# Kernel optimization log

Hardware: AMD Instinct MI355X
Metric: run time of the kernel (lower is better)

The kernel has to match this reference:

```python
import jax, jax.numpy as jnp
import numpy as np
import math

HIDDEN = 256

def setup_inputs() -> dict:
    key = jax.random.key(0)
    ks = jax.random.split(key, 4)
    x = jax.random.normal(ks[0], (64, 1024, 32), dtype=jnp.float32)
    Wq = jax.random.normal(ks[1], (32, HIDDEN), dtype=jnp.float32) * (1.0 / math.sqrt(32))
    Wk = jax.random.normal(ks[2], (32, HIDDEN), dtype=jnp.float32) * (1.0 / math.sqrt(32))
    Wv = jax.random.normal(ks[3], (32, HIDDEN), dtype=jnp.float32) * (1.0 / math.sqrt(32))
    bq = jnp.zeros((HIDDEN,), jnp.float32)
    bk = jnp.zeros((HIDDEN,), jnp.float32)
    bv = jnp.zeros((HIDDEN,), jnp.float32)
    return {"x": x, "Wq": Wq, "bq": bq, "Wk": Wk, "bk": bk, "Wv": Wv, "bv": bv}

def reference(x, Wq, bq, Wk, bk, Wv, bv):
    # per-sample single-head attention; softmax FIRST, then divide by sqrt(hidden)
    Q = jnp.einsum('bsi,ih->bsh', x, Wq) + bq  # [B,S,H]
    K = jnp.einsum('bsi,ih->bsh', x, Wk) + bk
    V = jnp.einsum('bsi,ih->bsh', x, Wv) + bv
    scores = jnp.einsum('bqh,bkh->bqk', Q, K)  # [B,S,S]
    attn = jax.nn.softmax(scores, axis=-1) / jnp.sqrt(jnp.float32(Q.shape[-1]))
    Z = jnp.einsum('bqk,bkh->bqh', attn, V)
    return Z
```

## Files before the change

### kernel.cpp

```cpp
#include <hip/hip_runtime.h>
#include <math.h>

#define NB   64
#define SEQ  1024
#define DIN  32
#define HID  256
#define QT   128
#define KT   64
#define NKT  (SEQ/KT)

typedef float        f32x16 __attribute__((ext_vector_type(16)));
typedef short        s16x8  __attribute__((ext_vector_type(8)));
typedef _Float16     f16x8  __attribute__((ext_vector_type(8)));
typedef unsigned int u32x4v __attribute__((ext_vector_type(4)));
typedef unsigned int u32x2v __attribute__((ext_vector_type(2)));

#define MFMA32(A,B,C)  __builtin_amdgcn_mfma_f32_32x32x16_bf16(A,B,C,0,0,0)
#define MFMA32H(A,B,C) __builtin_amdgcn_mfma_f32_32x32x16_f16(A,B,C,0,0,0)

#define OFF_WVT  4224
#define OFF_A    24576
#define OFF_T    (OFF_A + 64*16*8192)
#define WS_NEED  ((size_t)OFF_T + 64*16*4096)

#define SETB(g,p) (((g)*2+(p))*12288)
#define ATS_OFF   49152
#define SMEM_SZ   (ATS_OFF + 4224)

__device__ __forceinline__ unsigned pk_bf16(float lo, float hi) {
  unsigned r;
  asm("v_cvt_pk_bf16_f32 %0, %1, %2" : "=v"(r) : "v"(lo), "v"(hi));
  return r;
}
__device__ __forceinline__ unsigned pkh(float a, float b) {
  return __builtin_bit_cast(unsigned, __builtin_amdgcn_cvt_pkrtz(a, b));
}
__device__ __forceinline__ void plswap(unsigned &vdst, unsigned &vsrc) {
  u32x2v r = __builtin_amdgcn_permlane32_swap(vdst, vsrc, false, false);
  vdst = r[0]; vsrc = r[1];
}
__device__ __forceinline__ float cross_max(float v) {
  u32x2v r = __builtin_amdgcn_permlane32_swap(__float_as_uint(v), __float_as_uint(v), false, false);
  return fmaxf(__uint_as_float(r[0]), __uint_as_float(r[1]));
}
__device__ __forceinline__ float cross_add(float v) {
  u32x2v r = __builtin_amdgcn_permlane32_swap(__float_as_uint(v), __float_as_uint(v), false, false);
  return __uint_as_float(r[0]) + __uint_as_float(r[1]);
}
__device__ __forceinline__ s16x8 frag4(unsigned a, unsigned b, unsigned c, unsigned d) {
  u32x4v t; t[0]=a; t[1]=b; t[2]=c; t[3]=d;
  return __builtin_bit_cast(s16x8, t);
}
__device__ __forceinline__ f16x8 frag4h(unsigned a, unsigned b, unsigned c, unsigned d) {
  u32x4v t; t[0]=a; t[1]=b; t[2]=c; t[3]=d;
  return __builtin_bit_cast(f16x8, t);
}
__device__ __forceinline__ f16x8 ldh(const void* p) {
  return __builtin_bit_cast(f16x8, *(const u32x4v*)p);
}
__device__ __forceinline__ unsigned bf16_hi_bits(float f) {
  unsigned ux = __float_as_uint(f);
  return (ux + 0x7fffu + ((ux >> 16) & 1u)) >> 16;
}
__device__ __forceinline__ unsigned pack_h2(float a, float b) {
  _Float16 ha = (_Float16)a, hb = (_Float16)b;
  return (unsigned)__builtin_bit_cast(unsigned short, ha) |
         ((unsigned)__builtin_bit_cast(unsigned short, hb) << 16);
}


__global__ __launch_bounds__(256) void pack2_kernel(
    const float* __restrict__ x,
    const float* __restrict__ Wq, const float* __restrict__ Wk,
    const float* __restrict__ bq, const float* __restrict__ Wv,
    char* __restrict__ ws) {
  __shared__ float xs[64 * 33];
  const int bid = blockIdx.x;
  const int t   = threadIdx.x;
  if (bid < 1024) {
    const int b = bid >> 4, kt = bid & 15;
    {
      const int r = t >> 2, c = (t & 3) * 8;
      const float* src = x + ((size_t)(b*SEQ + kt*KT + r))*DIN + c;
      float4 v0 = *(const float4*)src, v1 = *(const float4*)(src + 4);
      float* d = xs + r*33 + c;
      d[0]=v0.x; d[1]=v0.y; d[2]=v0.z; d[3]=v0.w;
      d[4]=v1.x; d[5]=v1.y; d[6]=v1.z; d[7]=v1.w;
    }
    __syncthreads();
    const int l = t & 63, f = t >> 6;
    const int w = l >> 5, lq = l & 31;
    {
      const int row = ((f&2)?32:0) + lq;
      const int d0  = ((f&1)?16:0) + 8*w;
      const float* vsrc = xs + row*33 + d0;
      unsigned hi[4], lo[4];
      #pragma unroll
      for (int j = 0; j < 4; ++j) {
        float a = vsrc[2*j], c2 = vsrc[2*j+1];
        _Float16 ha = (_Float16)a, hb = (_Float16)c2;
        hi[j] = (unsigned)__builtin_bit_cast(unsigned short, ha) |
                ((unsigned)__builtin_bit_cast(unsigned short, hb) << 16);
        lo[j] = pack_h2(a - (float)ha, c2 - (float)hb);
      }
      char* dst = ws + OFF_A + (size_t)bid*8192 + f*1024 + l*16;
      *(u32x4v*)dst          = (u32x4v){hi[0],hi[1],hi[2],hi[3]};
      *(u32x4v*)(dst + 4096) = (u32x4v){lo[0],lo[1],lo[2],lo[3]};
    }
    {
      const int k0 = 16*f + 8*w;
      unsigned hi[4];
      #pragma unroll
      for (int j = 0; j < 4; ++j)
        hi[j] = pack_h2(xs[(k0 + 2*j)*33 + lq], xs[(k0 + 2*j + 1)*33 + lq]);
      char* dst = ws + OFF_T + (size_t)bid*4096 + f*1024 + l*16;
      *(u32x4v*)dst = (u32x4v){hi[0],hi[1],hi[2],hi[3]};
    }
  } else {
    const int gid = (bid - 1024) * 256 + t;
    float* wsf = (float*)ws;
    if (gid < 1024) {
      int i = gid >> 5, j = gid & 31;
      const float* a  = Wq + j * HID;
      const float* b2 = Wk + i * HID;
      float a0=0.f,a1=0.f,a2=0.f,a3=0.f;
      for (int h = 0; h < HID; h += 8) {
        float4 x1 = *(const float4*)(a + h),  y1 = *(const float4*)(b2 + h);
        float4 x2 = *(const float4*)(a + h+4), y2 = *(const float4*)(b2 + h+4);
        a0 = fmaf(x1.x,y1.x,a0); a1 = fmaf(x1.y,y1.y,a1);
        a2 = fmaf(x1.z,y1.z,a2); a3 = fmaf(x1.w,y1.w,a3);
        a0 = fmaf(x2.x,y2.x,a0); a1 = fmaf(x2.y,y2.y,a1);
        a2 = fmaf(x2.z,y2.z,a2); a3 = fmaf(x2.w,y2.w,a3);
      }
      wsf[gid] = (a0+a1)+(a2+a3);
    } else if (gid < 1056) {
      int i2 = gid - 1024;
      const float* b2 = Wk + i2 * HID;
      float acc = 0.f;
      for (int h = 0; h < HID; ++h) acc = fmaf(b2[h], bq[h], acc);
      wsf[1024 + i2] = acc;
    } else if (gid < 1056 + HID*16) {
      int e = gid - 1056;
      int h = e >> 4, d = e & 15;
      ((unsigned*)(ws + OFF_WVT))[e] = pkh(Wv[(2*d)*HID + h], Wv[(2*d+1)*HID + h]);
    }
  }
}

__global__ __launch_bounds__(512, 4) void attn_fast(
    const float* __restrict__ x, const char* __restrict__ ws,
    const float* __restrict__ bv, float* __restrict__ out) {
  __shared__ __align__(16) char smem[40960];
  const int bid = blockIdx.x;
  const int vid = (bid & 7) * 128 + (bid >> 3);
  const int b   = vid >> 4;
  const int q0  = (vid & 15) * 64;
  const int t = threadIdx.x;
  const int wid = t>>6, lane = t&63, w = lane>>5, lq = lane&31;
  const int grp = wid >> 1, wq = wid & 1;

  float* ATs = (float*)smem;
  {
    const float* wsf = (const float*)ws;
    for (int e = t; e < 1056; e += 512) ATs[e] = wsf[e];
  }
  __syncthreads();
  f16x8 G0h, G0l, G1h, G1l;
  {
    float xq[32];
    const float* xrow = x + (size_t)(b*SEQ + q0 + wq*32 + lq) * DIN;
    #pragma unroll
    for (int c = 0; c < 8; ++c) {
      float4 v = *(const float4*)(xrow + c*4);
      xq[c*4+0]=v.x; xq[c*4+1]=v.y; xq[c*4+2]=v.z; xq[c*4+3]=v.w;
    }
    float g[16];
    #pragma unroll
    for (int ii = 0; ii < 16; ++ii) {
      const int i = 8*w + 16*(ii>>3) + (ii&7);
      const float* ar = ATs + i*32;
      float acc = ATs[1024 + i];
      #pragma unroll
      for (int j = 0; j < 8; ++j) {
        float4 av = *(const float4*)(ar + j*4);
        acc = fmaf(xq[j*4+0], av.x, acc);
        acc = fmaf(xq[j*4+1], av.y, acc);
        acc = fmaf(xq[j*4+2], av.z, acc);
        acc = fmaf(xq[j*4+3], av.w, acc);
      }
      g[ii] = acc;
    }
    __syncthreads();
    unsigned gh[8], gl[8];
    #pragma unroll
    for (int p = 0; p < 8; ++p) {
      float a = g[2*p], bb = g[2*p+1];
      _Float16 ha = (_Float16)a, hb = (_Float16)bb;
      gh[p] = (unsigned)__builtin_bit_cast(unsigned short, ha) |
              ((unsigned)__builtin_bit_cast(unsigned short, hb) << 16);
      gl[p] = pack_h2(a - (float)ha, bb - (float)hb);
    }
    G0h = frag4h(gh[0],gh[1],gh[2],gh[3]);
    G1h = frag4h(gh[4],gh[5],gh[6],gh[7]);
    G0l = frag4h(gl[0],gl[1],gl[2],gl[3]);
    G1l = frag4h(gl[4],gl[5],gl[6],gl[7]);
  }

  f32x16 oacc;
  #pragma unroll
  for (int r = 0; r < 16; ++r) oacc[r] = 0.f;
  float m = -INFINITY, l = 0.f;

  const char* Ab = ws + OFF_A + (size_t)(b*16 + grp*4)*8192;
  const char* Tb = ws + OFF_T + (size_t)(b*16 + grp*4)*4096;
  const int lo16 = lane*16;

  #pragma unroll 2
  for (int j = 0; j < 4; ++j) {
    const char* A = Ab + j*8192;
    const char* T = Tb + j*4096;
    f16x8 ah0 = ldh(A + 0*1024 + lo16);
    f16x8 ah1 = ldh(A + 1*1024 + lo16);
    f16x8 ah2 = ldh(A + 2*1024 + lo16);
    f16x8 ah3 = ldh(A + 3*1024 + lo16);
    f16x8 al0 = ldh(A + 4096 + 0*1024 + lo16);
    f16x8 al1 = ldh(A + 4096 + 1*1024 + lo16);
    f16x8 al2 = ldh(A + 4096 + 2*1024 + lo16);
    f16x8 al3 = ldh(A + 4096 + 3*1024 + lo16);
    f16x8 at0 = ldh(T + 0*1024 + lo16);
    f16x8 at1 = ldh(T + 1*1024 + lo16);
    f16x8 at2 = ldh(T + 2*1024 + lo16);
    f16x8 at3 = ldh(T + 3*1024 + lo16);

    f32x16 sa0, sa1;
    #pragma unroll
    for (int r = 0; r < 16; ++r) { sa0[r] = 0.f; sa1[r] = 0.f; }
    sa0 = MFMA32H(ah0, G0h, sa0); sa0 = MFMA32H(ah0, G0l, sa0); sa0 = MFMA32H(al0, G0h, sa0);
    sa0 = MFMA32H(ah1, G1h, sa0); sa0 = MFMA32H(ah1, G1l, sa0); sa0 = MFMA32H(al1, G1h, sa0);
    sa1 = MFMA32H(ah2, G0h, sa1); sa1 = MFMA32H(ah2, G0l, sa1); sa1 = MFMA32H(al2, G0h, sa1);
    sa1 = MFMA32H(ah3, G1h, sa1); sa1 = MFMA32H(ah3, G1l, sa1); sa1 = MFMA32H(al3, G1h, sa1);

    float t0 = fmaxf(fmaxf(sa0[0], sa0[1]),  fmaxf(sa0[2],  sa0[3]));
    float t1 = fmaxf(fmaxf(sa0[4], sa0[5]),  fmaxf(sa0[6],  sa0[7]));
    float t2 = fmaxf(fmaxf(sa0[8], sa0[9]),  fmaxf(sa0[10], sa0[11]));
    float t3 = fmaxf(fmaxf(sa0[12],sa0[13]), fmaxf(sa0[14], sa0[15]));
    float t4 = fmaxf(fmaxf(sa1[0], sa1[1]),  fmaxf(sa1[2],  sa1[3]));
    float t5 = fmaxf(fmaxf(sa1[4], sa1[5]),  fmaxf(sa1[6],  sa1[7]));
    float t6 = fmaxf(fmaxf(sa1[8], sa1[9]),  fmaxf(sa1[10], sa1[11]));
    float t7 = fmaxf(fmaxf(sa1[12],sa1[13]), fmaxf(sa1[14], sa1[15]));
    float tm = fmaxf(fmaxf(fmaxf(t0,t1), fmaxf(t2,t3)),
                     fmaxf(fmaxf(t4,t5), fmaxf(t6,t7)));
    tm = cross_max(tm);
    if (!__all(tm - m <= 8.0f)) {
      float mn = fmaxf(m, tm);
      float alpha = __expf(m - mn);
      m = mn;
      l *= alpha;
      #pragma unroll
      for (int r = 0; r < 16; ++r) oacc[r] *= alpha;
    }
    #pragma unroll
    for (int r = 0; r < 16; ++r) { sa0[r] = __expf(sa0[r] - m); sa1[r] = __expf(sa1[r] - m); }
    float s0 = (sa0[0] + sa0[1])  + (sa0[2]  + sa0[3]);
    float s1 = (sa0[4] + sa0[5])  + (sa0[6]  + sa0[7]);
    float s2 = (sa0[8] + sa0[9])  + (sa0[10] + sa0[11]);
    float s3 = (sa0[12]+ sa0[13]) + (sa0[14] + sa0[15]);
    float s4 = (sa1[0] + sa1[1])  + (sa1[2]  + sa1[3]);
    float s5 = (sa1[4] + sa1[5])  + (sa1[6]  + sa1[7]);
    float s6 = (sa1[8] + sa1[9])  + (sa1[10] + sa1[11]);
    float s7 = (sa1[12]+ sa1[13]) + (sa1[14] + sa1[15]);
    float ps = ((s0+s1) + (s2+s3)) + ((s4+s5) + (s6+s7));
    ps = cross_add(ps);
    l += ps;

    {
      unsigned u0 = pkh(sa0[0], sa0[1]),  u1 = pkh(sa0[2], sa0[3]);
      unsigned v0 = pkh(sa0[4], sa0[5]),  v1 = pkh(sa0[6], sa0[7]);
      plswap(u0, v0); plswap(u1, v1);
      oacc = MFMA32H(at0, frag4h(u0, u1, v0, v1), oacc);

      unsigned u2 = pkh(sa0[8], sa0[9]),   u3 = pkh(sa0[10], sa0[11]);
      unsigned v2 = pkh(sa0[12], sa0[13]), v3 = pkh(sa0[14], sa0[15]);
      plswap(u2, v2); plswap(u3, v3);
      oacc = MFMA32H(at1, frag4h(u2, u3, v2, v3), oacc);

      unsigned u4 = pkh(sa1[0], sa1[1]),  u5 = pkh(sa1[2], sa1[3]);
      unsigned v4 = pkh(sa1[4], sa1[5]),  v5 = pkh(sa1[6], sa1[7]);
      plswap(u4, v4); plswap(u5, v5);
      oacc = MFMA32H(at2, frag4h(u4, u5, v4, v5), oacc);

      unsigned u6 = pkh(sa1[8], sa1[9]),   u7 = pkh(sa1[10], sa1[11]);
      unsigned v6 = pkh(sa1[12], sa1[13]), v7 = pkh(sa1[14], sa1[15]);
      plswap(u6, v6); plswap(u7, v7);
      oacc = MFMA32H(at3, frag4h(u6, u7, v6, v7), oacc);
    }
  }

  {
    float* ms = (float*)(smem + (((grp*2 + wq)<<6) | lane) * 80);
    *(float4*)(ms + 0)  = (float4){oacc[0],  oacc[1],  oacc[2],  oacc[3]};
    *(float4*)(ms + 4)  = (float4){oacc[4],  oacc[5],  oacc[6],  oacc[7]};
    *(float4*)(ms + 8)  = (float4){oacc[8],  oacc[9],  oacc[10], oacc[11]};
    *(float4*)(ms + 12) = (float4){oacc[12], oacc[13], oacc[14], oacc[15]};
    ms[16] = m; ms[17] = l;
    __syncthreads();
    #pragma unroll
    for (int og = 0; og < 4; ++og) {
      if (og == grp) continue;
      const float* pp = (const float*)(smem + (((og*2 + wq)<<6) | lane) * 80);
      float4 p0 = *(const float4*)(pp + 0);
      float4 p1 = *(const float4*)(pp + 4);
      float4 p2 = *(const float4*)(pp + 8);
      float4 p3 = *(const float4*)(pp + 12);
      float pm = pp[16], pl = pp[17];
      float mf = fmaxf(m, pm);
      float as = __expf(m - mf), ap = __expf(pm - mf);
      l = l * as + pl * ap;
      float po[16] = {p0.x,p0.y,p0.z,p0.w, p1.x,p1.y,p1.z,p1.w,
                      p2.x,p2.y,p2.z,p2.w, p3.x,p3.y,p3.z,p3.w};
      #pragma unroll
      for (int r = 0; r < 16; ++r) oacc[r] = oacc[r] * as + po[r] * ap;
      m = mf;
    }
    __syncthreads();
  }

  float inv = 1.0f / (16.0f * l);
  #pragma unroll
  for (int r = 0; r < 16; ++r) oacc[r] *= inv;
  f16x8 of0, of1;
  {
    unsigned u0 = pkh(oacc[0], oacc[1]),  u1 = pkh(oacc[2], oacc[3]);
    unsigned v0 = pkh(oacc[4], oacc[5]),  v1 = pkh(oacc[6], oacc[7]);
    plswap(u0, v0); plswap(u1, v1);
    of0 = frag4h(u0, u1, v0, v1);
    unsigned u2 = pkh(oacc[8], oacc[9]),   u3 = pkh(oacc[10], oacc[11]);
    unsigned v2 = pkh(oacc[12], oacc[13]), v3 = pkh(oacc[14], oacc[15]);
    plswap(u2, v2); plswap(u3, v3);
    of1 = frag4h(u2, u3, v2, v3);
  }
  const char* WvTb = ws + OFF_WVT;
  float* zb = (float*)(smem + wid * 4224);
  const size_t orow = ((size_t)b * SEQ + q0 + wq*32);
  #pragma unroll 1
  for (int mi = 0; mi < 2; ++mi) {
    const int mt = grp*2 + mi;
    const char* wp = WvTb + (mt*32 + lq)*64 + 16*w;
    f16x8 a0 = ldh(wp);
    f16x8 a1 = ldh(wp + 32);
    f32x16 z;
    #pragma unroll
    for (int r = 0; r < 16; ++r) z[r] = 0.f;
    z = MFMA32H(a0, of0, z);
    z = MFMA32H(a1, of1, z);
    #pragma unroll
    for (int r = 0; r < 16; ++r) {
      int hl = (r&3) + 8*(r>>2) + 4*w;
      zb[hl*33 + lq] = z[r];
    }
    asm volatile("s_waitcnt lgkmcnt(0)" ::: "memory");
    float bvv = bv[mt*32 + lq] * 0.0625f;
    #pragma unroll
    for (int jj = 0; jj < 16; ++jj) {
      int q = w*16 + jj;
      out[(orow + q)*HID + mt*32 + lq] = zb[lq*33 + q] + bvv;
    }
    asm volatile("s_waitcnt lgkmcnt(0)" ::: "memory");
  }
}


__global__ void precompute_kernel(const float* __restrict__ Wq, const float* __restrict__ Wk,
                                  const float* __restrict__ bq, const float* __restrict__ Wv,
                                  float* __restrict__ ws) {
  const int gid = blockIdx.x * 256 + threadIdx.x;
  if (gid < 1024) {
    int i = gid >> 5, j = gid & 31;
    const float* a  = Wq + j * HID;
    const float* b2 = Wk + i * HID;
    float a0=0.f,a1=0.f,a2=0.f,a3=0.f;
    for (int h = 0; h < HID; h += 8) {
      float4 x1 = *(const float4*)(a + h),  y1 = *(const float4*)(b2 + h);
      float4 x2 = *(const float4*)(a + h+4), y2 = *(const float4*)(b2 + h+4);
      a0 = fmaf(x1.x,y1.x,a0); a1 = fmaf(x1.y,y1.y,a1);
      a2 = fmaf(x1.z,y1.z,a2); a3 = fmaf(x1.w,y1.w,a3);
      a0 = fmaf(x2.x,y2.x,a0); a1 = fmaf(x2.y,y2.y,a1);
      a2 = fmaf(x2.z,y2.z,a2); a3 = fmaf(x2.w,y2.w,a3);
    }
    ws[gid] = (a0+a1)+(a2+a3);
  } else if (gid < 1056) {
    int i2 = gid - 1024;
    const float* b2 = Wk + i2 * HID;
    float acc = 0.f;
    for (int h = 0; h < HID; ++h) acc = fmaf(b2[h], bq[h], acc);
    ws[1024 + i2] = acc;
  } else if (gid < 1056 + HID*16) {
    int e = gid - 1056;
    int h = e >> 4, d = e & 15;
    ((unsigned*)((char*)ws + 4224))[e] = pk_bf16(Wv[(2*d)*HID + h], Wv[(2*d+1)*HID + h]);
  }
}

__global__ __launch_bounds__(512, 4) void attn_kernel(
    const float* __restrict__ x, const float* __restrict__ ws,
    const float* __restrict__ bv, float* __restrict__ out) {
  __shared__ __align__(16) char smem[SMEM_SZ];
  const int b    = blockIdx.y;
  const int q0   = blockIdx.x * QT;
  const int t    = threadIdx.x;
  const int grp  = t >> 8;
  const int ts   = t & 255;
  const int wid  = t >> 6;
  const int wq   = wid & 3;
  const int lane = t & 63;
  const int w    = lane >> 5;
  const int lq   = lane & 31;
  const float* xb = x + (size_t)b * SEQ * DIN;

  float* ATs = (float*)(smem + ATS_OFF);
  for (int e = t; e < 1056; e += 512) ATs[e] = ws[e];

  {
    const int sb = SETB(grp, 0);
    const int r = ts >> 2, s4 = ts & 3;
    const float* src = xb + (size_t)(grp * KT + r) * DIN + s4 * 8;
    float4 va = *(const float4*)src;
    float4 vb = *(const float4*)(src + 4);
    unsigned h0 = bf16_hi_bits(va.x) | (bf16_hi_bits(va.y) << 16);
    unsigned h1 = bf16_hi_bits(va.z) | (bf16_hi_bits(va.w) << 16);
    unsigned h2 = bf16_hi_bits(vb.x) | (bf16_hi_bits(vb.y) << 16);
    unsigned h3 = bf16_hi_bits(vb.z) | (bf16_hi_bits(vb.w) << 16);
    unsigned l0 = bf16_hi_bits(va.x - __uint_as_float(h0<<16)) | (bf16_hi_bits(va.y - __uint_as_float(h0 & 0xffff0000u)) << 16);
    unsigned l1 = bf16_hi_bits(va.z - __uint_as_float(h1<<16)) | (bf16_hi_bits(va.w - __uint_as_float(h1 & 0xffff0000u)) << 16);
    unsigned l2 = bf16_hi_bits(vb.x - __uint_as_float(h2<<16)) | (bf16_hi_bits(vb.y - __uint_as_float(h2 & 0xffff0000u)) << 16);
    unsigned l3 = bf16_hi_bits(vb.z - __uint_as_float(h3<<16)) | (bf16_hi_bits(vb.w - __uint_as_float(h3 & 0xffff0000u)) << 16);
    int off = r*64 + ((s4 ^ (r & 3)) << 4);
    *(u32x4v*)(smem + sb + off)        = (u32x4v){h0,h1,h2,h3};
    *(u32x4v*)(smem + sb + 4096 + off) = (u32x4v){l0,l1,l2,l3};
    const int ci = ts & 31, cr = (ts >> 5) * 8;
    const float* cs = xb + (size_t)(grp * KT + cr) * DIN + ci;
    float c0=cs[0], c1=cs[DIN], c2=cs[2*DIN], c3=cs[3*DIN];
    float c4=cs[4*DIN], c5=cs[5*DIN], c6=cs[6*DIN], c7=cs[7*DIN];
    unsigned t0 = pk_bf16(c0,c1), t1 = pk_bf16(c2,c3), t2 = pk_bf16(c4,c5), t3 = pk_bf16(c6,c7);
    int toff = sb + 8192 + ci*128 + (((ts>>5) ^ (ci & 7)) << 4);
    *(u32x4v*)(smem + toff) = (u32x4v){t0,t1,t2,t3};
  }
  __syncthreads();

  float g[16];
  {
    float xq[32];
    const float* xrow = xb + (size_t)(q0 + wq*32 + lq) * DIN;
    #pragma unroll
    for (int c = 0; c < 8; ++c) {
      float4 v = *(const float4*)(xrow + c*4);
      xq[c*4+0]=v.x; xq[c*4+1]=v.y; xq[c*4+2]=v.z; xq[c*4+3]=v.w;
    }
    #pragma unroll
    for (int ii = 0; ii < 16; ++ii) {
      const int i = 8*w + 16*(ii>>3) + (ii&7);
      const float* ar = ATs + i*32;
      float acc = ATs[1024 + i];
      #pragma unroll
      for (int j = 0; j < 8; ++j) {
        float4 av = *(const float4*)(ar + j*4);
        acc = fmaf(xq[j*4+0], av.x, acc);
        acc = fmaf(xq[j*4+1], av.y, acc);
        acc = fmaf(xq[j*4+2], av.z, acc);
        acc = fmaf(xq[j*4+3], av.w, acc);
      }
      g[ii] = acc;
    }
  }
  s16x8 G0h, G0l, G1h, G1l;
  {
    unsigned gh[2][4], gl[2][4];
    #pragma unroll
    for (int Ks = 0; Ks < 2; ++Ks)
      #pragma unroll
      for (int d = 0; d < 4; ++d) {
        float ga = g[Ks*8 + 2*d], gb = g[Ks*8 + 2*d + 1];
        unsigned hp = bf16_hi_bits(ga) | (bf16_hi_bits(gb) << 16);
        unsigned lp = bf16_hi_bits(ga - __uint_as_float(hp<<16)) |
                      (bf16_hi_bits(gb - __uint_as_float(hp & 0xffff0000u)) << 16);
        gh[Ks][d] = hp; gl[Ks][d] = lp;
      }
    G0h = frag4(gh[0][0],gh[0][1],gh[0][2],gh[0][3]);
    G0l = frag4(gl[0][0],gl[0][1],gl[0][2],gl[0][3]);
    G1h = frag4(gh[1][0],gh[1][1],gh[1][2],gh[1][3]);
    G1l = frag4(gl[1][0],gl[1][1],gl[1][2],gl[1][3]);
  }

  f32x16 oacc;
  #pragma unroll
  for (int r = 0; r < 16; ++r) oacc[r] = 0.f;
  float m = -INFINITY, l = 0.f;

  for (int j = 0; j < NKT/2; ++j) {
    const bool hn = (j + 1 < NKT/2);
    float4 va, vb;
    float c0=0,c1=0,c2=0,c3=0,c4=0,c5=0,c6=0,c7=0;
    if (hn) {
      const int ktn = 2*(j+1) + grp;
      const int r = ts >> 2, s4 = ts & 3;
      const float* src = xb + (size_t)(ktn*KT + r) * DIN + s4*8;
      va = *(const float4*)src;
      vb = *(const float4*)(src + 4);
      const int ci = ts & 31, cr = (ts >> 5) * 8;
      const float* cs = xb + (size_t)(ktn*KT + cr) * DIN + ci;
      c0=cs[0]; c1=cs[DIN]; c2=cs[2*DIN]; c3=cs[3*DIN];
      c4=cs[4*DIN]; c5=cs[5*DIN]; c6=cs[6*DIN]; c7=cs[7*DIN];
    }

    const int sb = SETB(grp, j & 1);
    const char* bh = smem + sb;
    const char* bl = smem + sb + 4096;
    const int co0 = ((w    ) ^ (lq & 3)) << 4;
    const int co1 = ((w + 2) ^ (lq & 3)) << 4;
    s16x8 ah00 = *(const s16x8*)(bh + lq*64 + co0);
    s16x8 ah01 = *(const s16x8*)(bh + lq*64 + co1);
    s16x8 al00 = *(const s16x8*)(bl + lq*64 + co0);
    s16x8 al01 = *(const s16x8*)(bl + lq*64 + co1);
    s16x8 ah10 = *(const s16x8*)(bh + (32+lq)*64 + co0);
    s16x8 ah11 = *(const s16x8*)(bh + (32+lq)*64 + co1);
    s16x8 al10 = *(const s16x8*)(bl + (32+lq)*64 + co0);
    s16x8 al11 = *(const s16x8*)(bl + (32+lq)*64 + co1);
    f32x16 sa0, sa1;
    #pragma unroll
    for (int r = 0; r < 16; ++r) { sa0[r] = 0.f; sa1[r] = 0.f; }
    sa0 = MFMA32(ah00, G0h, sa0); sa0 = MFMA32(ah00, G0l, sa0); sa0 = MFMA32(al00, G0h, sa0);
    sa0 = MFMA32(ah01, G1h, sa0); sa0 = MFMA32(ah01, G1l, sa0); sa0 = MFMA32(al01, G1h, sa0);
    sa1 = MFMA32(ah10, G0h, sa1); sa1 = MFMA32(ah10, G0l, sa1); sa1 = MFMA32(al10, G0h, sa1);
    sa1 = MFMA32(ah11, G1h, sa1); sa1 = MFMA32(ah11, G1l, sa1); sa1 = MFMA32(al11, G1h, sa1);

    float tm = sa0[0];
    #pragma unroll
    for (int r = 1; r < 16; ++r) tm = fmaxf(tm, sa0[r]);
    #pragma unroll
    for (int r = 0; r < 16; ++r) tm = fmaxf(tm, sa1[r]);
    tm = cross_max(tm);
    float mn = fmaxf(m, tm);
    float alpha = __expf(m - mn);
    m = mn;
    float ps = 0.f;
    #pragma unroll
    for (int r = 0; r < 16; ++r) { float p = __expf(sa0[r] - mn); sa0[r] = p; ps += p; }
    #pragma unroll
    for (int r = 0; r < 16; ++r) { float p = __expf(sa1[r] - mn); sa1[r] = p; ps += p; }
    ps = cross_add(ps);
    l = l * alpha + ps;
    #pragma unroll
    for (int r = 0; r < 16; ++r) oacc[r] *= alpha;

    const char* bt = smem + sb + 8192;
    {
      unsigned u0 = pk_bf16(sa0[0], sa0[1]),  u1 = pk_bf16(sa0[2], sa0[3]);
      unsigned v0 = pk_bf16(sa0[4], sa0[5]),  v1 = pk_bf16(sa0[6], sa0[7]);
      plswap(u0, v0); plswap(u1, v1);
      s16x8 at0 = *(const s16x8*)(bt + lq*128 + (((0 + w) ^ (lq & 7)) << 4));
      oacc = MFMA32(at0, frag4(u0, u1, v0, v1), oacc);

      unsigned u2 = pk_bf16(sa0[8], sa0[9]),   u3 = pk_bf16(sa0[10], sa0[11]);
      unsigned v2 = pk_bf16(sa0[12], sa0[13]), v3 = pk_bf16(sa0[14], sa0[15]);
      plswap(u2, v2); plswap(u3, v3);
      s16x8 at1 = *(const s16x8*)(bt + lq*128 + (((2 + w) ^ (lq & 7)) << 4));
      oacc = MFMA32(at1, frag4(u2, u3, v2, v3), oacc);

      unsigned u4 = pk_bf16(sa1[0], sa1[1]),  u5 = pk_bf16(sa1[2], sa1[3]);
      unsigned v4 = pk_bf16(sa1[4], sa1[5]),  v5 = pk_bf16(sa1[6], sa1[7]);
      plswap(u4, v4); plswap(u5, v5);
      s16x8 at2 = *(const s16x8*)(bt + lq*128 + (((4 + w) ^ (lq & 7)) << 4));
      oacc = MFMA32(at2, frag4(u4, u5, v4, v5), oacc);

      unsigned u6 = pk_bf16(sa1[8], sa1[9]),   u7 = pk_bf16(sa1[10], sa1[11]);
      unsigned v6 = pk_bf16(sa1[12], sa1[13]), v7 = pk_bf16(sa1[14], sa1[15]);
      plswap(u6, v6); plswap(u7, v7);
      s16x8 at3 = *(const s16x8*)(bt + lq*128 + (((6 + w) ^ (lq & 7)) << 4));
      oacc = MFMA32(at3, frag4(u6, u7, v6, v7), oacc);
    }

    if (hn) {
      const int nsb = SETB(grp, (j+1) & 1);
      const int r = ts >> 2, s4 = ts & 3;
      unsigned h0 = bf16_hi_bits(va.x) | (bf16_hi_bits(va.y) << 16);
      unsigned h1 = bf16_hi_bits(va.z) | (bf16_hi_bits(va.w) << 16);
      unsigned h2 = bf16_hi_bits(vb.x) | (bf16_hi_bits(vb.y) << 16);
      unsigned h3 = bf16_hi_bits(vb.z) | (bf16_hi_bits(vb.w) << 16);
      unsigned l0 = bf16_hi_bits(va.x - __uint_as_float(h0<<16)) | (bf16_hi_bits(va.y - __uint_as_float(h0 & 0xffff0000u)) << 16);
      unsigned l1 = bf16_hi_bits(va.z - __uint_as_float(h1<<16)) | (bf16_hi_bits(va.w - __uint_as_float(h1 & 0xffff0000u)) << 16);
      unsigned l2 = bf16_hi_bits(vb.x - __uint_as_float(h2<<16)) | (bf16_hi_bits(vb.y - __uint_as_float(h2 & 0xffff0000u)) << 16);
      unsigned l3 = bf16_hi_bits(vb.z - __uint_as_float(h3<<16)) | (bf16_hi_bits(vb.w - __uint_as_float(h3 & 0xffff0000u)) << 16);
      int off = r*64 + ((s4 ^ (r & 3)) << 4);
      *(u32x4v*)(smem + nsb + off)        = (u32x4v){h0,h1,h2,h3};
      *(u32x4v*)(smem + nsb + 4096 + off) = (u32x4v){l0,l1,l2,l3};
      const int ci = ts & 31;
      unsigned t0 = pk_bf16(c0,c1), t1 = pk_bf16(c2,c3), t2 = pk_bf16(c4,c5), t3 = pk_bf16(c6,c7);
      int toff = nsb + 8192 + ci*128 + (((ts>>5) ^ (ci & 7)) << 4);
      *(u32x4v*)(smem + toff) = (u32x4v){t0,t1,t2,t3};
    }
    __syncthreads();
  }

  {
    float* ms = (float*)(smem + grp*20480 + (((wq<<6) | lane) * 80));
    *(float4*)(ms + 0)  = (float4){oacc[0],  oacc[1],  oacc[2],  oacc[3]};
    *(float4*)(ms + 4)  = (float4){oacc[4],  oacc[5],  oacc[6],  oacc[7]};
    *(float4*)(ms + 8)  = (float4){oacc[8],  oacc[9],  oacc[10], oacc[11]};
    *(float4*)(ms + 12) = (float4){oacc[12], oacc[13], oacc[14], oacc[15]};
    ms[16] = m; ms[17] = l;
    __syncthreads();
    const float* pp = (const float*)(smem + (1-grp)*20480 + (((wq<<6) | lane) * 80));
    float4 p0 = *(const float4*)(pp + 0);
    float4 p1 = *(const float4*)(pp + 4);
    float4 p2 = *(const float4*)(pp + 8);
    float4 p3 = *(const float4*)(pp + 12);
    float pm = pp[16], pl = pp[17];
    float mf = fmaxf(m, pm);
    float as = __expf(m - mf), ap = __expf(pm - mf);
    l = l * as + pl * ap;
    float po[16] = {p0.x,p0.y,p0.z,p0.w, p1.x,p1.y,p1.z,p1.w,
                    p2.x,p2.y,p2.z,p2.w, p3.x,p3.y,p3.z,p3.w};
    #pragma unroll
    for (int r = 0; r < 16; ++r) oacc[r] = oacc[r] * as + po[r] * ap;
    __syncthreads();
  }

  float inv = 1.0f / (16.0f * l);
  #pragma unroll
  for (int r = 0; r < 16; ++r) oacc[r] *= inv;
  s16x8 of0, of1;
  {
    unsigned u0 = pk_bf16(oacc[0], oacc[1]),  u1 = pk_bf16(oacc[2], oacc[3]);
    unsigned v0 = pk_bf16(oacc[4], oacc[5]),  v1 = pk_bf16(oacc[6], oacc[7]);
    plswap(u0, v0); plswap(u1, v1);
    of0 = frag4(u0, u1, v0, v1);
    unsigned u2 = pk_bf16(oacc[8], oacc[9]),   u3 = pk_bf16(oacc[10], oacc[11]);
    unsigned v2 = pk_bf16(oacc[12], oacc[13]), v3 = pk_bf16(oacc[14], oacc[15]);
    plswap(u2, v2); plswap(u3, v3);
    of1 = frag4(u2, u3, v2, v3);
  }
  const char* WvTb = (const char*)ws + 4224;
  float* zb = (float*)(smem + wid * 4224);
  const size_t orow = ((size_t)b * SEQ + q0 + wq*32);
  #pragma unroll 1
  for (int mi = 0; mi < 4; ++mi) {
    const int mt = grp*4 + mi;
    const char* wp = WvTb + (mt*32 + lq)*64 + 16*w;
    s16x8 a0 = *(const s16x8*)wp;
    s16x8 a1 = *(const s16x8*)(wp + 32);
    f32x16 z;
    #pragma unroll
    for (int r = 0; r < 16; ++r) z[r] = 0.f;
    z = MFMA32(a0, of0, z);
    z = MFMA32(a1, of1, z);
    #pragma unroll
    for (int r = 0; r < 16; ++r) {
      int hl = (r&3) + 8*(r>>2) + 4*w;
      zb[hl*33 + lq] = z[r];
    }
    asm volatile("s_waitcnt lgkmcnt(0)" ::: "memory");
    float bvv = bv[mt*32 + lq] * 0.0625f;
    #pragma unroll
    for (int jj = 0; jj < 16; ++jj) {
      int q = w*16 + jj;
      out[(orow + q)*HID + mt*32 + lq] = zb[lq*33 + q] + bvv;
    }
    asm volatile("s_waitcnt lgkmcnt(0)" ::: "memory");
  }
}

extern "C" void kernel_launch(void* const* d_in, const int* in_sizes, int n_in,
                              void* d_out, int out_size, void* d_ws, size_t ws_size,
                              hipStream_t stream) {
  (void)in_sizes; (void)n_in; (void)out_size;
  const float* x  = (const float*)d_in[0];
  const float* Wq = (const float*)d_in[1];
  const float* bq = (const float*)d_in[2];
  const float* Wk = (const float*)d_in[3];
  const float* Wv = (const float*)d_in[5];
  const float* bv = (const float*)d_in[6];
  float* out = (float*)d_out;
  float* ws  = (float*)d_ws;

  if (ws_size >= WS_NEED) {
    pack2_kernel<<<1048, 256, 0, stream>>>(x, Wq, Wk, bq, Wv, (char*)ws);
    attn_fast<<<1024, 512, 0, stream>>>(x, (const char*)ws, bv, out);
  } else {
    precompute_kernel<<<24, 256, 0, stream>>>(Wq, Wk, bq, Wv, ws);
    attn_kernel<<<dim3(SEQ/QT, NB), 512, 0, stream>>>(x, ws, bv, out);
  }
}
```

Measured before the change: 68.87 us.

## Halve attention block to 32 queries, fold log2e into scores, share G via LDS

Each attn_fast block now handles 32 query rows with 4 waves (256 threads) instead of 64 rows with 8 waves, doubling the grid to 2048 blocks and halving shared memory. The per-query G projection is now computed cooperatively by all threads into a padded LDS buffer instead of redundantly per wave. The log2(e) factor is folded into the precomputed score matrix so softmax can use the native exp2 instead of __expf, and the rescale threshold is adjusted to match. The aim is better occupancy and load balance plus fewer ALU ops in the exponent, at the cost of an extra barrier and more blocks each rereading the keys from the workspace.

```diff
diff --git a/kernel.cpp b/kernel.cpp
--- a/kernel.cpp
+++ b/kernel.cpp
@@ -8,6 +8,7 @@
 #define QT   128
 #define KT   64
 #define NKT  (SEQ/KT)
+#define LOG2E 1.4426950408889634f
 
 typedef float        f32x16 __attribute__((ext_vector_type(16)));
 typedef short        s16x8  __attribute__((ext_vector_type(8)));
@@ -27,6 +28,9 @@
 #define ATS_OFF   49152
 #define SMEM_SZ   (ATS_OFF + 4224)
 
+__device__ __forceinline__ float ex2(float v) {
+  return __builtin_amdgcn_exp2f(v);
+}
 __device__ __forceinline__ unsigned pk_bf16(float lo, float hi) {
   unsigned r;
   asm("v_cvt_pk_bf16_f32 %0, %1, %2" : "=v"(r) : "v"(lo), "v"(hi));
@@ -132,13 +136,13 @@
         a0 = fmaf(x2.x,y2.x,a0); a1 = fmaf(x2.y,y2.y,a1);
         a2 = fmaf(x2.z,y2.z,a2); a3 = fmaf(x2.w,y2.w,a3);
       }
-      wsf[gid] = (a0+a1)+(a2+a3);
+      wsf[gid] = ((a0+a1)+(a2+a3)) * LOG2E;
     } else if (gid < 1056) {
       int i2 = gid - 1024;
       const float* b2 = Wk + i2 * HID;
       float acc = 0.f;
       for (int h = 0; h < HID; ++h) acc = fmaf(b2[h], bq[h], acc);
-      wsf[1024 + i2] = acc;
+      wsf[1024 + i2] = acc * LOG2E;
     } else if (gid < 1056 + HID*16) {
       int e = gid - 1056;
       int h = e >> 4, d = e & 15;
@@ -147,50 +151,54 @@
   }
 }
 
-__global__ __launch_bounds__(512, 4) void attn_fast(
+__global__ __launch_bounds__(256, 4) void attn_fast(
     const float* __restrict__ x, const char* __restrict__ ws,
     const float* __restrict__ bv, float* __restrict__ out) {
-  __shared__ __align__(16) char smem[40960];
+  __shared__ __align__(16) char smem[20480];
   const int bid = blockIdx.x;
-  const int vid = (bid & 7) * 128 + (bid >> 3);
-  const int b   = vid >> 4;
-  const int q0  = (vid & 15) * 64;
+  const int vid = (bid & 7) * 256 + (bid >> 3);
+  const int b   = vid >> 5;
+  const int q0  = (vid & 31) * 32;
   const int t = threadIdx.x;
   const int wid = t>>6, lane = t&63, w = lane>>5, lq = lane&31;
-  const int grp = wid >> 1, wq = wid & 1;
+  const int grp = wid;
 
   float* ATs = (float*)smem;
+  float* Gs  = (float*)(smem + 4480);
   {
     const float* wsf = (const float*)ws;
-    for (int e = t; e < 1056; e += 512) ATs[e] = wsf[e];
+    for (int e = t; e < 1024; e += 256) ATs[(e>>5)*33 + (e&31)] = wsf[e];
+    if (t < 32) ATs[1056 + t] = wsf[1024 + t];
   }
   __syncthreads();
-  f16x8 G0h, G0l, G1h, G1l;
-  {
+  {
+    const int q = t >> 3, i0 = (t & 7) * 4;
     float xq[32];
-    const float* xrow = x + (size_t)(b*SEQ + q0 + wq*32 + lq) * DIN;
+    const float* xrow = x + (size_t)(b*SEQ + q0 + q) * DIN;
     #pragma unroll
     for (int c = 0; c < 8; ++c) {
       float4 v = *(const float4*)(xrow + c*4);
       xq[c*4+0]=v.x; xq[c*4+1]=v.y; xq[c*4+2]=v.z; xq[c*4+3]=v.w;
     }
+    #pragma unroll
+    for (int jo = 0; jo < 4; ++jo) {
+      const int i = i0 + jo;
+      const float* ar = ATs + i*33;
+      float acc = ATs[1056 + i];
+      #pragma unroll
+      for (int j = 0; j < 32; ++j) acc = fmaf(xq[j], ar[j], acc);
+      Gs[q*33 + i] = acc;
+    }
+  }
+  __syncthreads();
+  f16x8 G0h, G0l, G1h, G1l;
+  {
     float g[16];
     #pragma unroll
     for (int ii = 0; ii < 16; ++ii) {
       const int i = 8*w + 16*(ii>>3) + (ii&7);
-      const float* ar = ATs + i*32;
-      float acc = ATs[1024 + i];
-      #pragma unroll
-      for (int j = 0; j < 8; ++j) {
-        float4 av = *(const float4*)(ar + j*4);
-        acc = fmaf(xq[j*4+0], av.x, acc);
-        acc = fmaf(xq[j*4+1], av.y, acc);
-        acc = fmaf(xq[j*4+2], av.z, acc);
-        acc = fmaf(xq[j*4+3], av.w, acc);
-      }
-      g[ii] = acc;
-    }
-    __syncthreads();
+      g[ii] = Gs[lq*33 + i];
+    }
     unsigned gh[8], gl[8];
     #pragma unroll
     for (int p = 0; p < 8; ++p) {
@@ -205,6 +213,7 @@
     G0l = frag4h(gl[0],gl[1],gl[2],gl[3]);
     G1l = frag4h(gl[4],gl[5],gl[6],gl[7]);
   }
+  __syncthreads();
 
   f32x16 oacc;
   #pragma unroll
@@ -251,16 +260,16 @@
     float tm = fmaxf(fmaxf(fmaxf(t0,t1), fmaxf(t2,t3)),
                      fmaxf(fmaxf(t4,t5), fmaxf(t6,t7)));
     tm = cross_max(tm);
-    if (!__all(tm - m <= 8.0f)) {
+    if (!__all(tm - m <= 11.5415603f)) {
       float mn = fmaxf(m, tm);
-      float alpha = __expf(m - mn);
+      float alpha = ex2(m - mn);
       m = mn;
       l *= alpha;
       #pragma unroll
       for (int r = 0; r < 16; ++r) oacc[r] *= alpha;
     }
     #pragma unroll
-    for (int r = 0; r < 16; ++r) { sa0[r] = __expf(sa0[r] - m); sa1[r] = __expf(sa1[r] - m); }
+    for (int r = 0; r < 16; ++r) { sa0[r] = ex2(sa0[r] - m); sa1[r] = ex2(sa1[r] - m); }
     float s0 = (sa0[0] + sa0[1])  + (sa0[2]  + sa0[3]);
     float s1 = (sa0[4] + sa0[5])  + (sa0[6]  + sa0[7]);
     float s2 = (sa0[8] + sa0[9])  + (sa0[10] + sa0[11]);
@@ -297,7 +306,7 @@
   }
 
   {
-    float* ms = (float*)(smem + (((grp*2 + wq)<<6) | lane) * 80);
+    float* ms = (float*)(smem + ((wid<<6) | lane) * 80);
     *(float4*)(ms + 0)  = (float4){oacc[0],  oacc[1],  oacc[2],  oacc[3]};
     *(float4*)(ms + 4)  = (float4){oacc[4],  oacc[5],  oacc[6],  oacc[7]};
     *(float4*)(ms + 8)  = (float4){oacc[8],  oacc[9],  oacc[10], oacc[11]};
@@ -306,15 +315,15 @@
     __syncthreads();
     #pragma unroll
     for (int og = 0; og < 4; ++og) {
-      if (og == grp) continue;
-      const float* pp = (const float*)(smem + (((og*2 + wq)<<6) | lane) * 80);
+      if (og == wid) continue;
+      const float* pp = (const float*)(smem + ((og<<6) | lane) * 80);
       float4 p0 = *(const float4*)(pp + 0);
       float4 p1 = *(const float4*)(pp + 4);
       float4 p2 = *(const float4*)(pp + 8);
       float4 p3 = *(const float4*)(pp + 12);
       float pm = pp[16], pl = pp[17];
       float mf = fmaxf(m, pm);
-      float as = __expf(m - mf), ap = __expf(pm - mf);
+      float as = ex2(m - mf), ap = ex2(pm - mf);
       l = l * as + pl * ap;
       float po[16] = {p0.x,p0.y,p0.z,p0.w, p1.x,p1.y,p1.z,p1.w,
                       p2.x,p2.y,p2.z,p2.w, p3.x,p3.y,p3.z,p3.w};
@@ -341,10 +350,10 @@
   }
   const char* WvTb = ws + OFF_WVT;
   float* zb = (float*)(smem + wid * 4224);
-  const size_t orow = ((size_t)b * SEQ + q0 + wq*32);
+  const size_t orow = ((size_t)b * SEQ + q0);
   #pragma unroll 1
   for (int mi = 0; mi < 2; ++mi) {
-    const int mt = grp*2 + mi;
+    const int mt = wid*2 + mi;
     const char* wp = WvTb + (mt*32 + lq)*64 + 16*w;
     f16x8 a0 = ldh(wp);
     f16x8 a1 = ldh(wp + 32);
@@ -684,7 +693,7 @@
 
   if (ws_size >= WS_NEED) {
     pack2_kernel<<<1048, 256, 0, stream>>>(x, Wq, Wk, bq, Wv, (char*)ws);
-    attn_fast<<<1024, 512, 0, stream>>>(x, (const char*)ws, bv, out);
+    attn_fast<<<2048, 256, 0, stream>>>(x, (const char*)ws, bv, out);
   } else {
     precompute_kernel<<<24, 256, 0, stream>>>(Wq, Wk, bq, Wv, ws);
     attn_kernel<<<dim3(SEQ/QT, NB), 512, 0, stream>>>(x, ws, bv, out);
```

New measurement: 58.06 us, median of 3. 1.19x faster.
